# Performance work log

Measured on AMD Instinct MI355X. Metric: run time of the kernel, lower is better.

## Reference

```python
import jax, jax.numpy as jnp
import numpy as np

N = 100000      # nodes
E = 1600000     # edges (avg degree 16)
ND = 64         # node feature dim (fiber degree-0 channels)
ED = 32         # edge feature dim
L = 3           # number of edge_update layers (num_layers - 1)
IN = ED + 2 * ND  # concat dim = 160
EPS = 1e-5
NEG_SLOPE = 0.01  # torch LeakyReLU default


def setup_inputs() -> dict:
    key = jax.random.key(0)
    ks = jax.random.split(key, 6)
    node_feat = jax.random.normal(ks[0], (N, ND), jnp.float32)
    edge_w = jax.random.normal(ks[1], (E, ED), jnp.float32)
    edge_i = jax.random.randint(ks[2], (E,), 0, N, jnp.int32)
    edge_j = jax.random.randint(ks[3], (E,), 0, N, jnp.int32)
    ln_g = jnp.ones((L, IN), jnp.float32)
    ln_b = jnp.zeros((L, IN), jnp.float32)
    w1 = jax.random.normal(ks[4], (L, IN, ED), jnp.float32) / np.sqrt(IN).astype(np.float32)
    b1 = jnp.zeros((L, ED), jnp.float32)
    w2 = jax.random.normal(ks[5], (L, ED, ED), jnp.float32) / np.sqrt(ED).astype(np.float32)
    b2 = jnp.zeros((L, ED), jnp.float32)
    return {"node_feat": node_feat, "edge_w": edge_w, "ln_g": ln_g, "ln_b": ln_b,
            "w1": w1, "b1": b1, "w2": w2, "b2": b2,
            "edge_i": edge_i, "edge_j": edge_j}


def _edge_update(nf, e, g, b, W1, B1, W2, B2, i, j):
    # gather per-edge endpoint features, concat with edge feature: [E, IN]
    x = jnp.concatenate([nf[i], nf[j], e], axis=-1)
    # LayerNorm over last dim
    mu = jnp.mean(x, axis=-1, keepdims=True)
    var = jnp.var(x, axis=-1, keepdims=True)
    x = (x - mu) * jax.lax.rsqrt(var + EPS) * g + b
    # Linear -> LeakyReLU -> Linear
    x = x @ W1 + B1
    x = jnp.where(x > 0, x, NEG_SLOPE * x)
    x = x @ W2 + B2
    return e + x  # residual edge update


def reference(node_feat, edge_w, ln_g, ln_b, w1, b1, w2, b2, edge_i, edge_j):
    e = edge_w
    for l in range(ln_g.shape[0]):  # small fixed layer count
        e = _edge_update(node_feat, e, ln_g[l], ln_b[l], w1[l], b1[l], w2[l], b2[l], edge_i, edge_j)
    return e
```

## Files before the change

### kernel.cpp

```cpp
#include <hip/hip_runtime.h>

#define EE     1600000
#define NN     100000
#define NDIM   64
#define EDIM   32
#define NLAYER 3
#define INDIM  160
#define TPB    256

static_assert(EE % TPB == 0, "grid must divide evenly");

__global__ __launch_bounds__(TPB) void node_precompute(
  const float* __restrict__ nf,  const float* __restrict__ lng,
  const float* __restrict__ lnb, const float* __restrict__ w1,
  const float* __restrict__ b1,
  float* __restrict__ P, float* __restrict__ nstat, float* __restrict__ cvec,
  float* __restrict__ wtab)
{
  __shared__ __align__(16) float sW[64*EDIM];
  __shared__ float sG[64];
  const int tid  = threadIdx.x;
  const int lp   = blockIdx.y;
  const int l    = lp >> 1, part = lp & 1;

  #pragma unroll
  for (int it = 0; it < 2; ++it){
    const int c = tid + it*TPB;
    const int d = c >> 3, ks = (c & 7) * 4;
    float4 v = *(const float4*)(w1 + (size_t)l*INDIM*EDIM + (size_t)(part*64 + d)*EDIM + ks);
    float* dst = &sW[d*EDIM + ks];
    dst[0]=v.x; dst[1]=v.y; dst[2]=v.z; dst[3]=v.w;
  }
  if (tid < 16){
    float4 v = *(const float4*)(lng + l*INDIM + part*64 + tid*4);
    sG[4*tid+0]=v.x; sG[4*tid+1]=v.y; sG[4*tid+2]=v.z; sG[4*tid+3]=v.w;
  }
  __syncthreads();

  if (lp == 0 && blockIdx.x == 0 && tid < 96){
    const int ll = tid >> 5, k = tid & 31;
    const float* wl = w1 + (size_t)ll*INDIM*EDIM;
    float c2 = 0.f, c1 = b1[ll*EDIM + k];
    for (int d = 0; d < INDIM; ++d){
      const float w = wl[d*EDIM + k];
      c2 = fmaf(lng[ll*INDIM + d], w, c2);
      c1 = fmaf(lnb[ll*INDIM + d], w, c1);
    }
    cvec[ll*EDIM + k]      = c2;
    cvec[96 + ll*EDIM + k] = c1;
  }
  if (lp == 1 && blockIdx.x == 0){
    #pragma unroll
    for (int it = 0; it < 12; ++it){
      const int c = tid + it*TPB;
      const int ll = c >> 10, rem = c & 1023;
      const int d = rem >> 5, k = rem & 31;
      wtab[c] = lng[ll*INDIM + 128 + d] * w1[(size_t)ll*INDIM*EDIM + (size_t)(128+d)*EDIM + k];
    }
  }

  const int n = blockIdx.x*TPB + tid;
  if (n >= NN) return;
  const float4* px = (const float4*)(nf + (size_t)n * NDIM);

  if (lp == 0){
    float s = 0.f, q = 0.f;
    #pragma unroll 1
    for (int c = 0; c < 16; ++c){
      float4 v = px[c];
      s += v.x + v.y + v.z + v.w;
      q = fmaf(v.x,v.x,q); q = fmaf(v.y,v.y,q);
      q = fmaf(v.z,v.z,q); q = fmaf(v.w,v.w,q);
    }
    nstat[2*n] = s; nstat[2*n+1] = q;
  }

  float acc[EDIM];
  #pragma unroll
  for (int k = 0; k < EDIM; ++k) acc[k] = 0.f;
  #pragma unroll 1
  for (int c = 0; c < 16; ++c){
    float4 xv = px[c];
    const float xs[4] = {xv.x, xv.y, xv.z, xv.w};
    const int d0 = 4*c;
    #pragma unroll
    for (int u = 0; u < 4; ++u){
      const float xd = xs[u] * sG[d0 + u];
      const float4* row = (const float4*)&sW[(size_t)(d0+u)*EDIM];
      #pragma unroll
      for (int q8 = 0; q8 < 8; ++q8){
        float4 w = row[q8];
        acc[4*q8+0] = fmaf(xd, w.x, acc[4*q8+0]);
        acc[4*q8+1] = fmaf(xd, w.y, acc[4*q8+1]);
        acc[4*q8+2] = fmaf(xd, w.z, acc[4*q8+2]);
        acc[4*q8+3] = fmaf(xd, w.w, acc[4*q8+3]);
      }
    }
  }
  float* dst = P + ((size_t)l*NN + n)*64 + part*EDIM;
  #pragma unroll
  for (int q8 = 0; q8 < 8; ++q8)
    ((float4*)dst)[q8] = make_float4(acc[4*q8+0], acc[4*q8+1], acc[4*q8+2], acc[4*q8+3]);
}

__global__ __launch_bounds__(TPB, 6) void edge_mlp_pre(
  const float* __restrict__ ew,
  const float* __restrict__ w2, const float* __restrict__ b2,
  const int* __restrict__ ei, const int* __restrict__ ej,
  const float* __restrict__ P, const float* __restrict__ nstat,
  const float* __restrict__ cvec, const float* __restrict__ wtab,
  float* __restrict__ out)
{
  __shared__ __align__(16) float sW1E[NLAYER*EDIM*EDIM];
  __shared__ __align__(16) float sW2 [NLAYER*EDIM*EDIM];
  __shared__ float sC2 [NLAYER*EDIM], sC1b[NLAYER*EDIM], sB2v[NLAYER*EDIM];

  const int tid = threadIdx.x;
  #pragma unroll
  for (int it = 0; it < 3; ++it){
    const int c = tid + it*TPB;
    ((float4*)sW1E)[c] = ((const float4*)wtab)[c];
  }
  #pragma unroll
  for (int it = 0; it < 3; ++it){
    const int c = tid + it*TPB;
    ((float4*)sW2)[c] = ((const float4*)w2)[c];
  }
  if (tid < 96){
    sC2 [tid] = cvec[tid];
    sC1b[tid] = cvec[96 + tid];
    sB2v[tid] = b2[tid];
  }
  __syncthreads();

  const int id = blockIdx.x * TPB + tid;
  const int i = ei[id], j = ej[id];

  const float2 sti = *(const float2*)(nstat + 2*(size_t)i);
  const float2 stj = *(const float2*)(nstat + 2*(size_t)j);
  const float sn = sti.x + stj.x, qn = sti.y + stj.y;

  float e[EDIM];
  {
    const float4* a = (const float4*)(ew + (size_t)id * EDIM);
    #pragma unroll
    for (int c = 0; c < 8; ++c){
      float4 v = a[c];
      e[4*c+0]=v.x; e[4*c+1]=v.y; e[4*c+2]=v.z; e[4*c+3]=v.w;
    }
  }

  const size_t iofs = (size_t)i * 64;
  const size_t jofs = (size_t)j * 64 + EDIM;

  #pragma unroll 1
  for (int l = 0; l < NLAYER; ++l){
    const float* Pl = P + (size_t)l * NN * 64;
    const float4* av = (const float4*)(Pl + iofs);
    const float4* bv = (const float4*)(Pl + jofs);

    float se = 0.f, qe = 0.f;
    #pragma unroll
    for (int d = 0; d < EDIM; ++d){
      se += e[d]; qe = fmaf(e[d], e[d], qe);
    }
    const float mu = (sn + se) * (1.f/INDIM);
    const float va = fmaxf(fmaf(-mu, mu, (qn + qe) * (1.f/INDIM)), 0.f);
    const float rs = rsqrtf(va + 1e-5f);
    const float nm = -mu * rs;

    float S[EDIM];
    #pragma unroll
    for (int c = 0; c < 8; ++c){
      float4 u = av[c], v = bv[c];
      S[4*c+0]=u.x+v.x; S[4*c+1]=u.y+v.y; S[4*c+2]=u.z+v.z; S[4*c+3]=u.w+v.w;
    }

    const float* wE = &sW1E[l*EDIM*EDIM];
    #pragma unroll
    for (int d = 0; d < EDIM; ++d){
      const float xd = e[d];
      const float4* row = (const float4*)(wE + d*EDIM);
      #pragma unroll
      for (int q = 0; q < 8; ++q){
        float4 w = row[q];
        S[4*q+0]=fmaf(xd,w.x,S[4*q+0]);
        S[4*q+1]=fmaf(xd,w.y,S[4*q+1]);
        S[4*q+2]=fmaf(xd,w.z,S[4*q+2]);
        S[4*q+3]=fmaf(xd,w.w,S[4*q+3]);
      }
    }

    const float* c2  = &sC2 [l*EDIM];
    const float* c1b = &sC1b[l*EDIM];
    const float* bb2 = &sB2v[l*EDIM];
    #pragma unroll
    for (int k = 0; k < EDIM; ++k){
      float a = fmaf(rs, S[k], fmaf(nm, c2[k], c1b[k]));
      S[k] = fmaxf(a, 0.01f*a);
    }
    #pragma unroll
    for (int k = 0; k < EDIM; ++k) e[k] += bb2[k];

    const float* w2l = &sW2[l*EDIM*EDIM];
    #pragma unroll
    for (int d = 0; d < EDIM; ++d){
      const float a = S[d];
      const float4* row = (const float4*)(w2l + d*EDIM);
      #pragma unroll
      for (int q = 0; q < 8; ++q){
        float4 w = row[q];
        e[4*q+0]=fmaf(a,w.x,e[4*q+0]);
        e[4*q+1]=fmaf(a,w.y,e[4*q+1]);
        e[4*q+2]=fmaf(a,w.z,e[4*q+2]);
        e[4*q+3]=fmaf(a,w.w,e[4*q+3]);
      }
    }
  }

  float4* o = (float4*)(out + (size_t)id * EDIM);
  #pragma unroll
  for (int c = 0; c < 8; ++c)
    o[c] = make_float4(e[4*c+0], e[4*c+1], e[4*c+2], e[4*c+3]);
}

#define EPT    2
#define EPB    (TPB*EPT)
static_assert(EE % EPB == 0, "grid must divide evenly");

__global__ __launch_bounds__(TPB, 2) void edge_mlp_fused(
  const float* __restrict__ nf,  const float* __restrict__ ew,
  const float* __restrict__ lng, const float* __restrict__ lnb,
  const float* __restrict__ w1,  const float* __restrict__ b1,
  const float* __restrict__ w2,  const float* __restrict__ b2,
  const int* __restrict__ ei, const int* __restrict__ ej,
  float* __restrict__ out)
{
  __shared__ float sW1[INDIM*EDIM];
  __shared__ float sW2[EDIM*EDIM];
  __shared__ float sC2[EDIM], sC1b[EDIM], sB2[EDIM];

  const int tid = threadIdx.x;
  const int id0 = blockIdx.x * EPB + tid;
  const int id1 = id0 + TPB;

  const float4* pi0 = (const float4*)(nf + (size_t)ei[id0] * NDIM);
  const float4* pj0 = (const float4*)(nf + (size_t)ej[id0] * NDIM);
  const float4* pi1 = (const float4*)(nf + (size_t)ei[id1] * NDIM);
  const float4* pj1 = (const float4*)(nf + (size_t)ej[id1] * NDIM);

  float e0[EDIM], e1[EDIM];
  {
    const float4* a = (const float4*)(ew + (size_t)id0 * EDIM);
    const float4* b = (const float4*)(ew + (size_t)id1 * EDIM);
    #pragma unroll
    for (int c = 0; c < 8; ++c){
      float4 v = a[c];
      e0[4*c+0]=v.x; e0[4*c+1]=v.y; e0[4*c+2]=v.z; e0[4*c+3]=v.w;
      float4 u = b[c];
      e1[4*c+0]=u.x; e1[4*c+1]=u.y; e1[4*c+2]=u.z; e1[4*c+3]=u.w;
    }
  }

  #pragma unroll 1
  for (int l = 0; l < NLAYER; ++l){
    __syncthreads();
    const float* w1l = w1 + (size_t)l * INDIM * EDIM;

    #pragma unroll
    for (int it = 0; it < 5; ++it){
      const int c = tid + it * TPB;
      const int d = c >> 3, ks = (c & 7) * 4;
      float4 v = *(const float4*)(w1l + d * EDIM + ks);
      const float g = lng[l * INDIM + d];
      sW1[d*EDIM+ks+0] = g*v.x; sW1[d*EDIM+ks+1] = g*v.y;
      sW1[d*EDIM+ks+2] = g*v.z; sW1[d*EDIM+ks+3] = g*v.w;
    }
    {
      const int d = tid >> 3, ks = (tid & 7) * 4;
      float4 v = *(const float4*)(w2 + (size_t)l*EDIM*EDIM + d*EDIM + ks);
      sW2[d*EDIM+ks+0] = v.x; sW2[d*EDIM+ks+1] = v.y;
      sW2[d*EDIM+ks+2] = v.z; sW2[d*EDIM+ks+3] = v.w;
    }
    if (tid < EDIM){
      float c1 = b1[l*EDIM + tid];
      for (int d = 0; d < INDIM; ++d)
        c1 = fmaf(lnb[l*INDIM + d], w1l[d*EDIM + tid], c1);
      sC1b[tid] = c1;
      sB2[tid]  = b2[l*EDIM + tid];
    }
    __syncthreads();
    if (tid < EDIM){
      float s = 0.f;
      for (int d = 0; d < INDIM; ++d) s += sW1[d*EDIM + tid];
      sC2[tid] = s;
    }
    __syncthreads();

    float S0[EDIM], S1[EDIM];
    #pragma unroll
    for (int k = 0; k < EDIM; ++k){ S0[k] = 0.f; S1[k] = 0.f; }
    float sum0 = 0.f, sq0 = 0.f, sum1 = 0.f, sq1 = 0.f;

    auto dot_row = [&](float xv0, float xv1, const float4* row){
      sum0 += xv0; sq0 = fmaf(xv0, xv0, sq0);
      sum1 += xv1; sq1 = fmaf(xv1, xv1, sq1);
      #pragma unroll
      for (int q = 0; q < 8; ++q){
        float4 w = row[q];
        S0[4*q+0] = fmaf(xv0, w.x, S0[4*q+0]); S1[4*q+0] = fmaf(xv1, w.x, S1[4*q+0]);
        S0[4*q+1] = fmaf(xv0, w.y, S0[4*q+1]); S1[4*q+1] = fmaf(xv1, w.y, S1[4*q+1]);
        S0[4*q+2] = fmaf(xv0, w.z, S0[4*q+2]); S1[4*q+2] = fmaf(xv1, w.z, S1[4*q+2]);
        S0[4*q+3] = fmaf(xv0, w.w, S0[4*q+3]); S1[4*q+3] = fmaf(xv1, w.w, S1[4*q+3]);
      }
    };

    #pragma unroll 1
    for (int c = 0; c < 32; ++c){
      const float4 x0 = (c < 16) ? pi0[c] : pj0[c - 16];
      const float4 x1 = (c < 16) ? pi1[c] : pj1[c - 16];
      const float4* wr = (const float4*)&sW1[c * 4 * EDIM];
      dot_row(x0.x, x1.x, wr + 0);
      dot_row(x0.y, x1.y, wr + 8);
      dot_row(x0.z, x1.z, wr + 16);
      dot_row(x0.w, x1.w, wr + 24);
    }
    #pragma unroll
    for (int d = 0; d < EDIM; ++d){
      const float4* row = (const float4*)&sW1[(2*NDIM + d) * EDIM];
      dot_row(e0[d], e1[d], row);
    }

    const float mu0 = sum0 * (1.f/INDIM);
    const float va0 = fmaxf(fmaf(-mu0, mu0, sq0 * (1.f/INDIM)), 0.f);
    const float rs0 = rsqrtf(va0 + 1e-5f);
    const float nm0 = -mu0 * rs0;
    const float mu1 = sum1 * (1.f/INDIM);
    const float va1 = fmaxf(fmaf(-mu1, mu1, sq1 * (1.f/INDIM)), 0.f);
    const float rs1 = rsqrtf(va1 + 1e-5f);
    const float nm1 = -mu1 * rs1;

    float h0[EDIM], h1v[EDIM];
    #pragma unroll
    for (int k = 0; k < EDIM; ++k){
      float a = fmaf(rs0, S0[k], fmaf(nm0, sC2[k], sC1b[k]));
      h0[k]  = fmaxf(a, 0.01f * a);
      float b = fmaf(rs1, S1[k], fmaf(nm1, sC2[k], sC1b[k]));
      h1v[k] = fmaxf(b, 0.01f * b);
    }
    #pragma unroll
    for (int k = 0; k < EDIM; ++k){ e0[k] += sB2[k]; e1[k] += sB2[k]; }
    #pragma unroll
    for (int d = 0; d < EDIM; ++d){
      const float a = h0[d], b = h1v[d];
      const float4* row = (const float4*)&sW2[d * EDIM];
      #pragma unroll
      for (int q = 0; q < 8; ++q){
        float4 w = row[q];
        e0[4*q+0] = fmaf(a, w.x, e0[4*q+0]); e1[4*q+0] = fmaf(b, w.x, e1[4*q+0]);
        e0[4*q+1] = fmaf(a, w.y, e0[4*q+1]); e1[4*q+1] = fmaf(b, w.y, e1[4*q+1]);
        e0[4*q+2] = fmaf(a, w.z, e0[4*q+2]); e1[4*q+2] = fmaf(b, w.z, e1[4*q+2]);
        e0[4*q+3] = fmaf(a, w.w, e0[4*q+3]); e1[4*q+3] = fmaf(b, w.w, e1[4*q+3]);
      }
    }
  }

  float4* o0 = (float4*)(out + (size_t)id0 * EDIM);
  float4* o1 = (float4*)(out + (size_t)id1 * EDIM);
  #pragma unroll
  for (int c = 0; c < 8; ++c){
    o0[c] = make_float4(e0[4*c+0], e0[4*c+1], e0[4*c+2], e0[4*c+3]);
    o1[c] = make_float4(e1[4*c+0], e1[4*c+1], e1[4*c+2], e1[4*c+3]);
  }
}

extern "C" void kernel_launch(void* const* d_in, const int* in_sizes, int n_in,
                              void* d_out, int out_size, void* d_ws, size_t ws_size,
                              hipStream_t stream)
{
  const float* nf  = (const float*)d_in[0];
  const float* ew  = (const float*)d_in[1];
  const float* lng = (const float*)d_in[2];
  const float* lnb = (const float*)d_in[3];
  const float* w1  = (const float*)d_in[4];
  const float* b1  = (const float*)d_in[5];
  const float* w2  = (const float*)d_in[6];
  const float* b2  = (const float*)d_in[7];
  const int*   ei  = (const int*)d_in[8];
  const int*   ej  = (const int*)d_in[9];
  float* out = (float*)d_out;

  const size_t PBYTES = (size_t)NLAYER * NN * 64 * sizeof(float);
  const size_t SBYTES = (size_t)NN * 2 * sizeof(float);
  const size_t CBYTES = (size_t)2 * NLAYER * EDIM * sizeof(float);
  const size_t WBYTES = (size_t)NLAYER * EDIM * EDIM * sizeof(float);

  if (d_ws && ws_size >= PBYTES + SBYTES + CBYTES + WBYTES){
    float* P     = (float*)d_ws;
    float* nstat = (float*)((char*)d_ws + PBYTES);
    float* cvec  = (float*)((char*)d_ws + PBYTES + SBYTES);
    float* wtab  = (float*)((char*)d_ws + PBYTES + SBYTES + CBYTES);
    hipLaunchKernelGGL(node_precompute,
                       dim3((NN + TPB - 1)/TPB, 6), dim3(TPB), 0, stream,
                       nf, lng, lnb, w1, b1, P, nstat, cvec, wtab);
    hipLaunchKernelGGL(edge_mlp_pre, dim3(EE / TPB), dim3(TPB), 0, stream,
                       ew, w2, b2, ei, ej, P, nstat, cvec, wtab, out);
  } else {
    dim3 grid(EE / EPB), block(TPB);
    hipLaunchKernelGGL(edge_mlp_fused, grid, block, 0, stream,
                       nf, ew, lng, lnb, w1, b1, w2, b2, ei, ej, out);
  }
}
```

Before: 997.4 us.

## Split each edge pair across two lanes with DPP half-swaps

The per-edge MLP kernel now assigns each pair of adjacent lanes to two edges, with each lane owning half of the 32 output channels for both edges. Partial LayerNorm sums and the other half of the input vector are exchanged with a DPP quad-permute (xor 1). Each LDS weight read now feeds two edges, which halves shared-memory traffic per FMA, and gathers of P rows become split half-rows per lane. The cost is that occupancy hints drop from 6 to 3 waves, and the DPP moves add instructions.

New measurement: 984.3 us. Within noise of the previous version (-1.3%).

```diff
diff --git a/kernel.cpp b/kernel.cpp
--- a/kernel.cpp
+++ b/kernel.cpp
@@ -9,6 +9,10 @@
 #define TPB    256
 
 static_assert(EE % TPB == 0, "grid must divide evenly");
+
+__device__ __forceinline__ float xor1f(float x){
+  return __int_as_float(__builtin_amdgcn_mov_dpp(__float_as_int(x), 0xB1, 0xF, 0xF, true));
+}
 
 __global__ __launch_bounds__(TPB) void node_precompute(
   const float* __restrict__ nf,  const float* __restrict__ lng,
@@ -103,7 +107,7 @@
     ((float4*)dst)[q8] = make_float4(acc[4*q8+0], acc[4*q8+1], acc[4*q8+2], acc[4*q8+3]);
 }
 
-__global__ __launch_bounds__(TPB, 6) void edge_mlp_pre(
+__global__ __launch_bounds__(TPB, 3) void edge_mlp_pair(
   const float* __restrict__ ew,
   const float* __restrict__ w2, const float* __restrict__ b2,
   const int* __restrict__ ei, const int* __restrict__ ej,
@@ -113,18 +117,16 @@
 {
   __shared__ __align__(16) float sW1E[NLAYER*EDIM*EDIM];
   __shared__ __align__(16) float sW2 [NLAYER*EDIM*EDIM];
-  __shared__ float sC2 [NLAYER*EDIM], sC1b[NLAYER*EDIM], sB2v[NLAYER*EDIM];
+  __shared__ __align__(16) float sC2 [NLAYER*EDIM];
+  __shared__ __align__(16) float sC1b[NLAYER*EDIM];
+  __shared__ __align__(16) float sB2v[NLAYER*EDIM];
 
   const int tid = threadIdx.x;
   #pragma unroll
   for (int it = 0; it < 3; ++it){
     const int c = tid + it*TPB;
     ((float4*)sW1E)[c] = ((const float4*)wtab)[c];
-  }
-  #pragma unroll
-  for (int it = 0; it < 3; ++it){
-    const int c = tid + it*TPB;
-    ((float4*)sW2)[c] = ((const float4*)w2)[c];
+    ((float4*)sW2 )[c] = ((const float4*)w2)[c];
   }
   if (tid < 96){
     sC2 [tid] = cvec[tid];
@@ -133,95 +135,163 @@
   }
   __syncthreads();
 
-  const int id = blockIdx.x * TPB + tid;
-  const int i = ei[id], j = ej[id];
-
-  const float2 sti = *(const float2*)(nstat + 2*(size_t)i);
-  const float2 stj = *(const float2*)(nstat + 2*(size_t)j);
-  const float sn = sti.x + stj.x, qn = sti.y + stj.y;
-
-  float e[EDIM];
+  const int p    = tid & 1;
+  const int kofs = p << 4;
+  const int id0  = blockIdx.x * TPB + ((tid >> 1) << 1);
+  const int id1  = id0 + 1;
+
+  const int i0 = ei[id0], j0 = ej[id0];
+  const int i1 = ei[id1], j1 = ej[id1];
+
+  const float2 sti0 = *(const float2*)(nstat + 2*(size_t)i0);
+  const float2 stj0 = *(const float2*)(nstat + 2*(size_t)j0);
+  const float2 sti1 = *(const float2*)(nstat + 2*(size_t)i1);
+  const float2 stj1 = *(const float2*)(nstat + 2*(size_t)j1);
+  const float sn0 = sti0.x + stj0.x, qn0 = sti0.y + stj0.y;
+  const float sn1 = sti1.x + stj1.x, qn1 = sti1.y + stj1.y;
+
+  float eo0[16], eo1[16];
   {
-    const float4* a = (const float4*)(ew + (size_t)id * EDIM);
-    #pragma unroll
-    for (int c = 0; c < 8; ++c){
-      float4 v = a[c];
-      e[4*c+0]=v.x; e[4*c+1]=v.y; e[4*c+2]=v.z; e[4*c+3]=v.w;
-    }
-  }
-
-  const size_t iofs = (size_t)i * 64;
-  const size_t jofs = (size_t)j * 64 + EDIM;
+    const float4* a0 = (const float4*)(ew + (size_t)id0 * EDIM + kofs);
+    const float4* a1 = (const float4*)(ew + (size_t)id1 * EDIM + kofs);
+    #pragma unroll
+    for (int q = 0; q < 4; ++q){
+      float4 v = a0[q];
+      eo0[4*q+0]=v.x; eo0[4*q+1]=v.y; eo0[4*q+2]=v.z; eo0[4*q+3]=v.w;
+      float4 u = a1[q];
+      eo1[4*q+0]=u.x; eo1[4*q+1]=u.y; eo1[4*q+2]=u.z; eo1[4*q+3]=u.w;
+    }
+  }
 
   #pragma unroll 1
   for (int l = 0; l < NLAYER; ++l){
-    const float* Pl = P + (size_t)l * NN * 64;
-    const float4* av = (const float4*)(Pl + iofs);
-    const float4* bv = (const float4*)(Pl + jofs);
-
-    float se = 0.f, qe = 0.f;
-    #pragma unroll
-    for (int d = 0; d < EDIM; ++d){
-      se += e[d]; qe = fmaf(e[d], e[d], qe);
-    }
-    const float mu = (sn + se) * (1.f/INDIM);
-    const float va = fmaxf(fmaf(-mu, mu, (qn + qe) * (1.f/INDIM)), 0.f);
-    const float rs = rsqrtf(va + 1e-5f);
-    const float nm = -mu * rs;
-
-    float S[EDIM];
-    #pragma unroll
-    for (int c = 0; c < 8; ++c){
-      float4 u = av[c], v = bv[c];
-      S[4*c+0]=u.x+v.x; S[4*c+1]=u.y+v.y; S[4*c+2]=u.z+v.z; S[4*c+3]=u.w+v.w;
-    }
-
-    const float* wE = &sW1E[l*EDIM*EDIM];
-    #pragma unroll
-    for (int d = 0; d < EDIM; ++d){
-      const float xd = e[d];
-      const float4* row = (const float4*)(wE + d*EDIM);
-      #pragma unroll
-      for (int q = 0; q < 8; ++q){
-        float4 w = row[q];
-        S[4*q+0]=fmaf(xd,w.x,S[4*q+0]);
-        S[4*q+1]=fmaf(xd,w.y,S[4*q+1]);
-        S[4*q+2]=fmaf(xd,w.z,S[4*q+2]);
-        S[4*q+3]=fmaf(xd,w.w,S[4*q+3]);
-      }
-    }
-
-    const float* c2  = &sC2 [l*EDIM];
-    const float* c1b = &sC1b[l*EDIM];
-    const float* bb2 = &sB2v[l*EDIM];
-    #pragma unroll
-    for (int k = 0; k < EDIM; ++k){
-      float a = fmaf(rs, S[k], fmaf(nm, c2[k], c1b[k]));
-      S[k] = fmaxf(a, 0.01f*a);
-    }
-    #pragma unroll
-    for (int k = 0; k < EDIM; ++k) e[k] += bb2[k];
+    const float* Pl = P + (size_t)l * (NN*64);
+    const float4* gi0 = (const float4*)(Pl + (size_t)i0*64 + kofs);
+    const float4* gj0 = (const float4*)(Pl + (size_t)j0*64 + 32 + kofs);
+    const float4* gi1 = (const float4*)(Pl + (size_t)i1*64 + kofs);
+    const float4* gj1 = (const float4*)(Pl + (size_t)j1*64 + 32 + kofs);
+
+    float4 gA0[4], gB0[4], gA1[4], gB1[4];
+    #pragma unroll
+    for (int q = 0; q < 4; ++q){
+      gA0[q] = gi0[q]; gB0[q] = gj0[q];
+      gA1[q] = gi1[q]; gB1[q] = gj1[q];
+    }
+
+    float sp0=0.f, qp0=0.f, sp1=0.f, qp1=0.f;
+    #pragma unroll
+    for (int m = 0; m < 16; ++m){
+      sp0 += eo0[m]; qp0 = fmaf(eo0[m], eo0[m], qp0);
+      sp1 += eo1[m]; qp1 = fmaf(eo1[m], eo1[m], qp1);
+    }
+    const float se0 = sp0 + xor1f(sp0), qe0 = qp0 + xor1f(qp0);
+    const float se1 = sp1 + xor1f(sp1), qe1 = qp1 + xor1f(qp1);
+
+    const float mu0 = (sn0 + se0) * (1.f/INDIM);
+    const float va0 = fmaxf(fmaf(-mu0, mu0, (qn0 + qe0) * (1.f/INDIM)), 0.f);
+    const float rs0 = rsqrtf(va0 + 1e-5f);
+    const float nm0 = -mu0 * rs0;
+    const float mu1 = (sn1 + se1) * (1.f/INDIM);
+    const float va1 = fmaxf(fmaf(-mu1, mu1, (qn1 + qe1) * (1.f/INDIM)), 0.f);
+    const float rs1 = rsqrtf(va1 + 1e-5f);
+    const float nm1 = -mu1 * rs1;
+
+    float S0[16], S1[16];
+    #pragma unroll
+    for (int m = 0; m < 16; ++m){ S0[m] = 0.f; S1[m] = 0.f; }
+    const float* wl = &sW1E[l*EDIM*EDIM];
+    #pragma unroll
+    for (int m = 0; m < 16; ++m){
+      const float x0 = eo0[m], x1 = eo1[m];
+      const float4* row = (const float4*)(wl + (kofs + m)*EDIM + kofs);
+      #pragma unroll
+      for (int q = 0; q < 4; ++q){
+        float4 w = row[q];
+        S0[4*q+0]=fmaf(x0,w.x,S0[4*q+0]); S1[4*q+0]=fmaf(x1,w.x,S1[4*q+0]);
+        S0[4*q+1]=fmaf(x0,w.y,S0[4*q+1]); S1[4*q+1]=fmaf(x1,w.y,S1[4*q+1]);
+        S0[4*q+2]=fmaf(x0,w.z,S0[4*q+2]); S1[4*q+2]=fmaf(x1,w.z,S1[4*q+2]);
+        S0[4*q+3]=fmaf(x0,w.w,S0[4*q+3]); S1[4*q+3]=fmaf(x1,w.w,S1[4*q+3]);
+      }
+    }
+    #pragma unroll
+    for (int m = 0; m < 16; ++m){
+      const float x0 = xor1f(eo0[m]), x1 = xor1f(eo1[m]);
+      const float4* row = (const float4*)(wl + ((kofs ^ 16) + m)*EDIM + kofs);
+      #pragma unroll
+      for (int q = 0; q < 4; ++q){
+        float4 w = row[q];
+        S0[4*q+0]=fmaf(x0,w.x,S0[4*q+0]); S1[4*q+0]=fmaf(x1,w.x,S1[4*q+0]);
+        S0[4*q+1]=fmaf(x0,w.y,S0[4*q+1]); S1[4*q+1]=fmaf(x1,w.y,S1[4*q+1]);
+        S0[4*q+2]=fmaf(x0,w.z,S0[4*q+2]); S1[4*q+2]=fmaf(x1,w.z,S1[4*q+2]);
+        S0[4*q+3]=fmaf(x0,w.w,S0[4*q+3]); S1[4*q+3]=fmaf(x1,w.w,S1[4*q+3]);
+      }
+    }
+
+    #pragma unroll
+    for (int q = 0; q < 4; ++q){
+      S0[4*q+0] += gA0[q].x + gB0[q].x; S1[4*q+0] += gA1[q].x + gB1[q].x;
+      S0[4*q+1] += gA0[q].y + gB0[q].y; S1[4*q+1] += gA1[q].y + gB1[q].y;
+      S0[4*q+2] += gA0[q].z + gB0[q].z; S1[4*q+2] += gA1[q].z + gB1[q].z;
+      S0[4*q+3] += gA0[q].w + gB0[q].w; S1[4*q+3] += gA1[q].w + gB1[q].w;
+    }
+
+    const float4* c2v = (const float4*)(&sC2 [l*EDIM + kofs]);
+    const float4* c1v = (const float4*)(&sC1b[l*EDIM + kofs]);
+    const float4* b2v = (const float4*)(&sB2v[l*EDIM + kofs]);
+    #pragma unroll
+    for (int q = 0; q < 4; ++q){
+      const float4 c2 = c2v[q], c1 = c1v[q], bb = b2v[q];
+      float a;
+      a = fmaf(rs0,S0[4*q+0],fmaf(nm0,c2.x,c1.x)); S0[4*q+0]=fmaxf(a,0.01f*a);
+      a = fmaf(rs1,S1[4*q+0],fmaf(nm1,c2.x,c1.x)); S1[4*q+0]=fmaxf(a,0.01f*a);
+      a = fmaf(rs0,S0[4*q+1],fmaf(nm0,c2.y,c1.y)); S0[4*q+1]=fmaxf(a,0.01f*a);
+      a = fmaf(rs1,S1[4*q+1],fmaf(nm1,c2.y,c1.y)); S1[4*q+1]=fmaxf(a,0.01f*a);
+      a = fmaf(rs0,S0[4*q+2],fmaf(nm0,c2.z,c1.z)); S0[4*q+2]=fmaxf(a,0.01f*a);
+      a = fmaf(rs1,S1[4*q+2],fmaf(nm1,c2.z,c1.z)); S1[4*q+2]=fmaxf(a,0.01f*a);
+      a = fmaf(rs0,S0[4*q+3],fmaf(nm0,c2.w,c1.w)); S0[4*q+3]=fmaxf(a,0.01f*a);
+      a = fmaf(rs1,S1[4*q+3],fmaf(nm1,c2.w,c1.w)); S1[4*q+3]=fmaxf(a,0.01f*a);
+      eo0[4*q+0]+=bb.x; eo1[4*q+0]+=bb.x;
+      eo0[4*q+1]+=bb.y; eo1[4*q+1]+=bb.y;
+      eo0[4*q+2]+=bb.z; eo1[4*q+2]+=bb.z;
+      eo0[4*q+3]+=bb.w; eo1[4*q+3]+=bb.w;
+    }
 
     const float* w2l = &sW2[l*EDIM*EDIM];
     #pragma unroll
-    for (int d = 0; d < EDIM; ++d){
-      const float a = S[d];
-      const float4* row = (const float4*)(w2l + d*EDIM);
-      #pragma unroll
-      for (int q = 0; q < 8; ++q){
-        float4 w = row[q];
-        e[4*q+0]=fmaf(a,w.x,e[4*q+0]);
-        e[4*q+1]=fmaf(a,w.y,e[4*q+1]);
-        e[4*q+2]=fmaf(a,w.z,e[4*q+2]);
-        e[4*q+3]=fmaf(a,w.w,e[4*q+3]);
-      }
-    }
-  }
-
-  float4* o = (float4*)(out + (size_t)id * EDIM);
-  #pragma unroll
-  for (int c = 0; c < 8; ++c)
-    o[c] = make_float4(e[4*c+0], e[4*c+1], e[4*c+2], e[4*c+3]);
+    for (int m = 0; m < 16; ++m){
+      const float a0 = S0[m], a1 = S1[m];
+      const float4* row = (const float4*)(w2l + (kofs + m)*EDIM + kofs);
+      #pragma unroll
+      for (int q = 0; q < 4; ++q){
+        float4 w = row[q];
+        eo0[4*q+0]=fmaf(a0,w.x,eo0[4*q+0]); eo1[4*q+0]=fmaf(a1,w.x,eo1[4*q+0]);
+        eo0[4*q+1]=fmaf(a0,w.y,eo0[4*q+1]); eo1[4*q+1]=fmaf(a1,w.y,eo1[4*q+1]);
+        eo0[4*q+2]=fmaf(a0,w.z,eo0[4*q+2]); eo1[4*q+2]=fmaf(a1,w.z,eo1[4*q+2]);
+        eo0[4*q+3]=fmaf(a0,w.w,eo0[4*q+3]); eo1[4*q+3]=fmaf(a1,w.w,eo1[4*q+3]);
+      }
+    }
+    #pragma unroll
+    for (int m = 0; m < 16; ++m){
+      const float a0 = xor1f(S0[m]), a1 = xor1f(S1[m]);
+      const float4* row = (const float4*)(w2l + ((kofs ^ 16) + m)*EDIM + kofs);
+      #pragma unroll
+      for (int q = 0; q < 4; ++q){
+        float4 w = row[q];
+        eo0[4*q+0]=fmaf(a0,w.x,eo0[4*q+0]); eo1[4*q+0]=fmaf(a1,w.x,eo1[4*q+0]);
+        eo0[4*q+1]=fmaf(a0,w.y,eo0[4*q+1]); eo1[4*q+1]=fmaf(a1,w.y,eo1[4*q+1]);
+        eo0[4*q+2]=fmaf(a0,w.z,eo0[4*q+2]); eo1[4*q+2]=fmaf(a1,w.z,eo1[4*q+2]);
+        eo0[4*q+3]=fmaf(a0,w.w,eo0[4*q+3]); eo1[4*q+3]=fmaf(a1,w.w,eo1[4*q+3]);
+      }
+    }
+  }
+
+  float4* o0 = (float4*)(out + (size_t)id0 * EDIM + kofs);
+  float4* o1 = (float4*)(out + (size_t)id1 * EDIM + kofs);
+  #pragma unroll
+  for (int q = 0; q < 4; ++q){
+    o0[q] = make_float4(eo0[4*q+0], eo0[4*q+1], eo0[4*q+2], eo0[4*q+3]);
+    o1[q] = make_float4(eo1[4*q+0], eo1[4*q+1], eo1[4*q+2], eo1[4*q+3]);
+  }
 }
 
 #define EPT    2
@@ -403,7 +473,7 @@
     hipLaunchKernelGGL(node_precompute,
                        dim3((NN + TPB - 1)/TPB, 6), dim3(TPB), 0, stream,
                        nf, lng, lnb, w1, b1, P, nstat, cvec, wtab);
-    hipLaunchKernelGGL(edge_mlp_pre, dim3(EE / TPB), dim3(TPB), 0, stream,
+    hipLaunchKernelGGL(edge_mlp_pair, dim3(EE / TPB), dim3(TPB), 0, stream,
                        ew, w2, b2, ei, ej, P, nstat, cvec, wtab, out);
   } else {
     dim3 grid(EE / EPB), block(TPB);
```
